# Optimization experiments

Measured on AMD Instinct MI355X. Metric: run time of the kernel, lower is better.

The kernel has to match this reference:

```python
import jax, jax.numpy as jnp
import numpy as np

D_MODEL = 1024
EPS = 1e-6

def setup_inputs() -> dict:
    key = jax.random.key(0)
    ks = jax.random.split(key, 13)
    B, T, S, E = 4, 2048, 2048, D_MODEL
    s = 1.0 / np.sqrt(E)
    return {
        "query": jax.random.normal(ks[0], (B, T, E), jnp.float32),
        "key": jax.random.normal(ks[1], (B, S, E), jnp.float32),
        "value": jax.random.normal(ks[2], (B, S, E), jnp.float32),
        "Wq": jax.random.normal(ks[3], (E, E), jnp.float32) * s,
        "bq": jax.random.normal(ks[4], (E,), jnp.float32) * 0.01,
        "Wk": jax.random.normal(ks[5], (E, E), jnp.float32) * s,
        "bk": jax.random.normal(ks[6], (E,), jnp.float32) * 0.01,
        "Wv": jax.random.normal(ks[7], (E, E), jnp.float32) * s,
        "bv": jax.random.normal(ks[8], (E,), jnp.float32) * 0.01,
        "Wo": jax.random.normal(ks[9], (E, E), jnp.float32) * s,
        "bo": jax.random.normal(ks[10], (E,), jnp.float32) * 0.01,
        "gamma": jnp.ones((E,), jnp.float32),
        "beta": jnp.zeros((E,), jnp.float32),
    }

def reference(query, key, value, Wq, bq, Wk, bk, Wv, bv, Wo, bo, gamma, beta):
    # Note: despite the name, the original never splits heads; attention is
    # over the full d_model with scale 1/sqrt(d_model). Dropout = eval identity.
    residual = query
    q = jnp.einsum('bte,fe->btf', query, Wq) + bq   # nn.Linear: x @ W.T + b
    k = jnp.einsum('bse,fe->bsf', key, Wk) + bk
    v = jnp.einsum('bse,fe->bsf', value, Wv) + bv
    scores = jnp.einsum('bte,bse->bts', q, k) / jnp.sqrt(jnp.float32(D_MODEL))
    attn = jax.nn.softmax(scores, axis=-1)          # (B, T, S)
    ctx = jnp.einsum('bts,bse->bte', attn, v)
    out = jnp.einsum('bte,fe->btf', ctx, Wo) + bo
    out = out + residual
    mu = jnp.mean(out, axis=-1, keepdims=True)
    var = jnp.mean(jnp.square(out - mu), axis=-1, keepdims=True)
    return (out - mu) * jax.lax.rsqrt(var + EPS) * gamma + beta
```

## Files before the change

### kernel.cpp

```cpp
#include <hip/hip_runtime.h>
#include <hip/hip_bf16.h>

typedef __bf16 bf16_t;
typedef __bf16 bf16x4 __attribute__((ext_vector_type(4)));
typedef __bf16 bf16x8 __attribute__((ext_vector_type(8)));
typedef float f32x4 __attribute__((ext_vector_type(4)));

#define E_DIM 1024
#define SEQ   2048
#define NBATCH 4

#define BARR()  asm volatile("s_barrier" ::: "memory")
#define LGKM0() asm volatile("s_waitcnt lgkmcnt(0)" ::: "memory")
#define VMC6()  asm volatile("s_waitcnt vmcnt(6)" ::: "memory")
#define VMC0()  asm volatile("s_waitcnt vmcnt(0)" ::: "memory")

__global__ __launch_bounds__(256) void k_cast2(
    const float* __restrict__ q, const float* __restrict__ k, const float* __restrict__ v,
    const float* __restrict__ wq, const float* __restrict__ wk,
    const float* __restrict__ wv, const float* __restrict__ wo,
    bf16_t* __restrict__ xq, bf16_t* __restrict__ xk, bf16_t* __restrict__ xv,
    bf16_t* __restrict__ wqb, bf16_t* __restrict__ wkb,
    bf16_t* __restrict__ wvb, bf16_t* __restrict__ wob) {
  const int b = blockIdx.x;
  const float* s; bf16_t* d; long base;
  if (b < 2048)        { s = q;  d = xq;  base = (long)b * 4096; }
  else if (b < 4096)   { s = k;  d = xk;  base = (long)(b - 2048) * 4096; }
  else if (b < 6144)   { s = v;  d = xv;  base = (long)(b - 4096) * 4096; }
  else if (b < 6400)   { s = wq; d = wqb; base = (long)(b - 6144) * 4096; }
  else if (b < 6656)   { s = wk; d = wkb; base = (long)(b - 6400) * 4096; }
  else if (b < 6912)   { s = wv; d = wvb; base = (long)(b - 6656) * 4096; }
  else                 { s = wo; d = wob; base = (long)(b - 6912) * 4096; }
  const long i = base + threadIdx.x * 16;
  const f32x4 a0 = *(const f32x4*)(s + i);
  const f32x4 a1 = *(const f32x4*)(s + i + 4);
  const f32x4 a2 = *(const f32x4*)(s + i + 8);
  const f32x4 a3 = *(const f32x4*)(s + i + 12);
  bf16x8 o0, o1;
#pragma unroll
  for (int j = 0; j < 4; ++j) {
    o0[j] = (bf16_t)a0[j]; o0[4 + j] = (bf16_t)a1[j];
    o1[j] = (bf16_t)a2[j]; o1[4 + j] = (bf16_t)a3[j];
  }
  *(bf16x8*)(d + i) = o0;
  *(bf16x8*)(d + i + 8) = o1;
}

template <int OUTMODE, bool RS, bool QKV3, int REPS, int NTL>
__global__ __launch_bounds__(256, 2) void k_g13(
    const bf16_t* __restrict__ A, int lda, long sA,
    const bf16_t* __restrict__ B, int ldb, long sB,
    void* __restrict__ Cv, int ldc, long sC,
    float scale, const float* __restrict__ bias,
    const float* __restrict__ residual, int GM, int GN,
    const bf16_t* __restrict__ A1, const bf16_t* __restrict__ A2,
    const bf16_t* __restrict__ B1, const bf16_t* __restrict__ B2,
    const float* __restrict__ bias1, const float* __restrict__ bias2,
    void* __restrict__ Cv1, void* __restrict__ Cv2) {
  constexpr int ASZ   = 16384;
  constexpr int BUFSZ = 32768;
  constexpr int NT    = 1 << NTL;
  constexpr int TT    = REPS << NTL;
  extern __shared__ char smem[];

  const int tid  = threadIdx.x;
  const int lane = tid & 63;
  const int wid  = tid >> 6;
  const int wm   = wid >> 1;
  const int wn   = wid & 1;
  const int l15  = lane & 15;
  const int lq   = lane >> 4;

  const int nwg  = gridDim.x;
  const int orig = blockIdx.x;
  const int wg   = (orig & 7) * (nwg >> 3) + (orig >> 3);

  const int colk = ((tid & 7) ^ ((tid >> 3) & 7)) << 3;
  const int trow = tid >> 3;
  const int ldsw = wid << 10;

  const bf16_t *pA0, *pB0, *pA1 = nullptr, *pB1 = nullptr, *pA2 = nullptr, *pB2 = nullptr;
  int zzr0 = 0, bmr0 = 0, bnr0 = 0, zzr1 = 0, bmr1 = 0, bnr1 = 0;
  if constexpr (QKV3) {
    bmr0 = wg / GN; bnr0 = wg - bmr0 * GN;
    const long aoff = (long)(bmr0 * 128 + trow) * lda + colk;
    const long boff = (long)(bnr0 * 128 + trow) * ldb + colk;
    pA0 = A + aoff;  pA1 = A1 + aoff;  pA2 = A2 + aoff;
    pB0 = B + boff;  pB1 = B1 + boff;  pB2 = B2 + boff;
  } else {
    {
      const int g  = wg;
      zzr0 = g / (GM * GN);
      const int rm = g - zzr0 * (GM * GN);
      bmr0 = rm / GN; bnr0 = rm - bmr0 * GN;
      pA0 = A + zzr0 * sA + (long)(bmr0 * 128 + trow) * lda + colk;
      pB0 = B + zzr0 * sB + (long)(bnr0 * 128 + trow) * ldb + colk;
    }
    if constexpr (REPS >= 2) {
      const int g  = nwg + wg;
      zzr1 = g / (GM * GN);
      const int rm = g - zzr1 * (GM * GN);
      bmr1 = rm / GN; bnr1 = rm - bmr1 * GN;
      pA1 = A + zzr1 * sA + (long)(bmr1 * 128 + trow) * lda + colk;
      pB1 = B + zzr1 * sB + (long)(bnr1 * 128 + trow) * ldb + colk;
    }
  }

#define GLL(gaddr, ldsoff)                                                       \
  __builtin_amdgcn_global_load_lds(                                             \
      (const __attribute__((address_space(1))) void*)(gaddr),                   \
      (__attribute__((address_space(3))) void*)(smem + (ldsoff)), 16, 0, 0)

  auto stA = [&](int tau, int buf) {
    tau = tau < TT ? tau : TT - 1;
    const int rep = tau >> NTL;
    const bf16_t* p = (REPS == 1) ? pA0
                    : (REPS == 2) ? (rep ? pA1 : pA0)
                    : (rep == 0 ? pA0 : (rep == 1 ? pA1 : pA2));
    p += (long)(tau & (NT - 1)) * 64;
#pragma unroll
    for (int s = 0; s < 4; ++s)
      GLL(p + (long)(s * 32) * lda, buf * BUFSZ + s * 4096 + ldsw);
  };
  auto stB = [&](int tau, int buf, int half) {
    tau = tau < TT ? tau : TT - 1;
    const int rep = tau >> NTL;
    const bf16_t* p = (REPS == 1) ? pB0
                    : (REPS == 2) ? (rep ? pB1 : pB0)
                    : (rep == 0 ? pB0 : (rep == 1 ? pB1 : pB2));
    p += (long)(tau & (NT - 1)) * 64;
#pragma unroll
    for (int s = 0; s < 2; ++s)
      GLL(p + (long)(half * 64 + s * 32) * ldb,
          buf * BUFSZ + ASZ + half * 8192 + s * 4096 + ldsw);
  };

  f32x4 acc[4][4];
#pragma unroll
  for (int m = 0; m < 4; ++m)
#pragma unroll
    for (int n = 0; n < 4; ++n) acc[m][n] = (f32x4){0.f, 0.f, 0.f, 0.f};
  f32x4 rs[4];
#pragma unroll
  for (int m = 0; m < 4; ++m) rs[m] = (f32x4){0.f, 0.f, 0.f, 0.f};
  bf16x8 vones;
#pragma unroll
  for (int i = 0; i < 8; ++i) vones[i] = (bf16_t)1.0f;

  auto ldA = [&](bf16x8 (&a)[2][2], int cur, int mq) {
#pragma unroll
    for (int i = 0; i < 2; ++i) {
      const int row = wm * 64 + (mq * 2 + i) * 16 + l15;
#pragma unroll
      for (int kk = 0; kk < 2; ++kk) {
        const int byt = cur * BUFSZ + row * 128 + ((kk * 64 + lq * 16) ^ ((row & 7) << 4));
        a[i][kk] = *(const bf16x8*)(smem + byt);
      }
    }
  };
  auto ldB = [&](bf16x8 (&b)[2][2], int cur, int nq) {
#pragma unroll
    for (int n2 = 0; n2 < 2; ++n2) {
      const int row = wn * 64 + (nq * 2 + n2) * 16 + l15;
#pragma unroll
      for (int kk = 0; kk < 2; ++kk) {
        const int byt = cur * BUFSZ + ASZ + row * 128 + ((kk * 64 + lq * 16) ^ ((row & 7) << 4));
        b[n2][kk] = *(const bf16x8*)(smem + byt);
      }
    }
  };
  auto mmaq = [&](bf16x8 (&a)[2][2], bf16x8 (&b)[2][2], int mq, int nq) {
    __builtin_amdgcn_s_setprio(1);
#pragma unroll
    for (int kk = 0; kk < 2; ++kk)
#pragma unroll
      for (int i = 0; i < 2; ++i)
#pragma unroll
        for (int n2 = 0; n2 < 2; ++n2)
          acc[mq * 2 + i][nq * 2 + n2] = __builtin_amdgcn_mfma_f32_16x16x32_bf16(
              a[i][kk], b[n2][kk], acc[mq * 2 + i][nq * 2 + n2], 0, 0, 0);
    __builtin_amdgcn_s_setprio(0);
  };
  auto mmars = [&](bf16x8 (&a)[2][2], int mq) {
#pragma unroll
    for (int kk = 0; kk < 2; ++kk)
#pragma unroll
      for (int i = 0; i < 2; ++i)
        rs[mq * 2 + i] = __builtin_amdgcn_mfma_f32_16x16x32_bf16(
            a[i][kk], vones, rs[mq * 2 + i], 0, 0, 0);
  };

  stB(0, 0, 0); stB(0, 0, 1); stA(0, 0);
  stB(1, 1, 0); stA(1, 1);
  VMC6();
  BARR();

  bf16x8 a0[2][2], a1[2][2], b0[2][2], b1[2][2];
  auto tile = [&](int t, int cur) {
    ldA(a0, cur, 0); ldB(b0, cur, 0);
    stB(t + 1, cur ^ 1, 1);
    BARR(); LGKM0();
    mmaq(a0, b0, 0, 0);
    BARR();
    ldB(b1, cur, 1);
    BARR(); LGKM0();
    mmaq(a0, b1, 0, 1);
    if constexpr (RS) mmars(a0, 0);
    BARR();
    ldA(a1, cur, 1);
    stB(t + 2, cur, 0);
    BARR(); LGKM0();
    mmaq(a1, b1, 1, 1);
    BARR();
    stA(t + 2, cur);
    BARR();
    mmaq(a1, b0, 1, 0);
    if constexpr (RS) mmars(a1, 1);
    VMC6();
    BARR();
  };

#pragma unroll
  for (int rep = 0; rep < REPS; ++rep) {
    const int tb = rep << NTL;
    for (int tt = 0; tt < NT; tt += 2) {
      tile(tb + tt, 0);
      tile(tb + tt + 1, 1);
    }

    {
      int zz2, bm2, bn2;
      const float* biasp;
      void* Cvp;
      bool tr = false;
      if constexpr (QKV3) {
        zz2 = 0; bm2 = bmr0; bn2 = bnr0;
        biasp = rep == 0 ? bias : (rep == 1 ? bias1 : bias2);
        Cvp   = rep == 0 ? Cv   : (rep == 1 ? Cv1   : Cv2);
        tr = (rep == 2);
      } else {
        zz2 = (REPS >= 2 && rep) ? zzr1 : zzr0;
        bm2 = (REPS >= 2 && rep) ? bmr1 : bmr0;
        bn2 = (REPS >= 2 && rep) ? bnr1 : bnr0;
        biasp = bias; Cvp = Cv;
      }
      const int colb = bn2 * 128 + wn * 64 + l15;
      const int rowb = bm2 * 128 + wm * 64 + lq * 4;
#pragma unroll
      for (int m = 0; m < 4; ++m) {
        float inv[4];
        if constexpr (RS) {
#pragma unroll
          for (int j = 0; j < 4; ++j) inv[j] = 1.0f / rs[m][j];
        }
#pragma unroll
        for (int n = 0; n < 4; ++n) {
          const int colg = colb + n * 16;
          float bval = 0.0f;
          if constexpr (OUTMODE != 3) bval = biasp ? biasp[colg] : 0.0f;
          if (QKV3 && tr) {
            const int r0 = rowb + m * 16;
            bf16x4 pk;
#pragma unroll
            for (int j = 0; j < 4; ++j) pk[j] = (bf16_t)(acc[m][n][j] * scale + bval);
            const long bb = (long)(r0 >> 11);
            const int ss = r0 & (SEQ - 1);
            *(bf16x4*)((bf16_t*)Cvp + bb * ((long)E_DIM * SEQ) + (long)colg * SEQ + ss) = pk;
          } else {
#pragma unroll
            for (int j = 0; j < 4; ++j) {
              const int r = rowb + m * 16 + j;
              float v;
              if constexpr (OUTMODE == 3) v = __expf(acc[m][n][j] * scale);
              else v = acc[m][n][j] * scale + bval;
              if constexpr (RS) v *= inv[j];
              if (OUTMODE == 0 && residual) v += residual[(long)r * ldc + colg];
              const long idx = (long)zz2 * sC + (long)r * ldc + colg;
              if constexpr (OUTMODE == 0) ((float*)Cvp)[idx] = v;
              else ((bf16_t*)Cvp)[idx] = (bf16_t)v;
            }
          }
        }
      }
      if (rep + 1 < REPS) {
#pragma unroll
        for (int m = 0; m < 4; ++m) {
#pragma unroll
          for (int n = 0; n < 4; ++n) acc[m][n] = (f32x4){0.f, 0.f, 0.f, 0.f};
          rs[m] = (f32x4){0.f, 0.f, 0.f, 0.f};
        }
      }
    }
  }
  VMC0();
#undef GLL
}

__global__ __launch_bounds__(256) void k_layernorm(float* __restrict__ out,
                                                   const float* __restrict__ gamma,
                                                   const float* __restrict__ beta) {
  const long row = blockIdx.x;
  float* rp = out + row * 1024;
  const int t = threadIdx.x;
  const float4 v = *(const float4*)(rp + t * 4);
  float s = v.x + v.y + v.z + v.w;
#pragma unroll
  for (int o = 32; o; o >>= 1) s += __shfl_xor(s, o);
  __shared__ float red1[4], red2[4];
  const int lane = t & 63, w = t >> 6;
  if (lane == 0) red1[w] = s;
  __syncthreads();
  const float mu = (red1[0] + red1[1] + red1[2] + red1[3]) * (1.0f / 1024.0f);
  const float d0 = v.x - mu, d1 = v.y - mu, d2 = v.z - mu, d3 = v.w - mu;
  float ss = d0 * d0 + d1 * d1 + d2 * d2 + d3 * d3;
#pragma unroll
  for (int o = 32; o; o >>= 1) ss += __shfl_xor(ss, o);
  if (lane == 0) red2[w] = ss;
  __syncthreads();
  const float var = (red2[0] + red2[1] + red2[2] + red2[3]) * (1.0f / 1024.0f);
  const float rsq = rsqrtf(var + 1e-6f);
  const float4 g = *(const float4*)(gamma + t * 4);
  const float4 b = *(const float4*)(beta + t * 4);
  float4 o;
  o.x = d0 * rsq * g.x + b.x;
  o.y = d1 * rsq * g.y + b.y;
  o.z = d2 * rsq * g.z + b.z;
  o.w = d3 * rsq * g.w + b.w;
  *(float4*)(rp + t * 4) = o;
}

extern "C" void kernel_launch(void* const* d_in, const int* in_sizes, int n_in,
                              void* d_out, int out_size, void* d_ws, size_t ws_size,
                              hipStream_t stream) {
  const float* query = (const float*)d_in[0];
  const float* key   = (const float*)d_in[1];
  const float* value = (const float*)d_in[2];
  const float* Wq = (const float*)d_in[3];
  const float* bq = (const float*)d_in[4];
  const float* Wk = (const float*)d_in[5];
  const float* bk = (const float*)d_in[6];
  const float* Wv = (const float*)d_in[7];
  const float* bv = (const float*)d_in[8];
  const float* Wo = (const float*)d_in[9];
  const float* bo = (const float*)d_in[10];
  const float* gamma = (const float*)d_in[11];
  const float* beta  = (const float*)d_in[12];
  float* out = (float*)d_out;

  char* ws = (char*)d_ws;
  const size_t XSZ = (size_t)NBATCH * SEQ * E_DIM * 2;
  const size_t WSZ = (size_t)E_DIM * E_DIM * 2;
  const size_t B2  = 3 * XSZ;

  bf16_t* Xq  = (bf16_t*)(ws + 0);
  bf16_t* Xk  = (bf16_t*)(ws + XSZ);
  bf16_t* Xv  = (bf16_t*)(ws + 2 * XSZ);
  bf16_t* SC  = (bf16_t*)(ws + 0);
  bf16_t* Wqb = (bf16_t*)(ws + B2);
  bf16_t* Wkb = (bf16_t*)(ws + B2 + WSZ);
  bf16_t* Wvb = (bf16_t*)(ws + B2 + 2 * WSZ);
  bf16_t* Wob = (bf16_t*)(ws + B2 + 3 * WSZ);
  bf16_t* Qb  = (bf16_t*)(ws + B2 + 4 * WSZ);
  bf16_t* Kb  = (bf16_t*)(ws + B2 + 4 * WSZ + XSZ);
  bf16_t* Vt  = (bf16_t*)(ws + B2 + 4 * WSZ + 2 * XSZ);
  bf16_t* Ctx = (bf16_t*)(ws + B2 + 4 * WSZ + 3 * XSZ);

  const int NTOK = NBATCH * SEQ;
  const int SMB = 65536;

  hipFuncSetAttribute((const void*)k_g13<1, false, true, 3, 4>, hipFuncAttributeMaxDynamicSharedMemorySize, SMB);
  hipFuncSetAttribute((const void*)k_g13<3, false, false, 2, 4>, hipFuncAttributeMaxDynamicSharedMemorySize, SMB);
  hipFuncSetAttribute((const void*)k_g13<1, true, false, 1, 5>, hipFuncAttributeMaxDynamicSharedMemorySize, SMB);
  hipFuncSetAttribute((const void*)k_g13<0, false, false, 1, 4>, hipFuncAttributeMaxDynamicSharedMemorySize, SMB);

  k_cast2<<<dim3(7168), 256, 0, stream>>>(query, key, value, Wq, Wk, Wv, Wo,
                                          Xq, Xk, Xv, Wqb, Wkb, Wvb, Wob);

  k_g13<1, false, true, 3, 4><<<512, 256, SMB, stream>>>(
      Xq, E_DIM, 0, Wqb, E_DIM, 0, Qb, E_DIM, 0, 1.0f, bq, nullptr, 64, 8,
      Xk, Xv, Wkb, Wvb, bk, bv, Kb, Vt);

  k_g13<3, false, false, 2, 4><<<512, 256, SMB, stream>>>(
      Qb, E_DIM, (long)SEQ * E_DIM, Kb, E_DIM, (long)SEQ * E_DIM,
      SC, SEQ, (long)SEQ * SEQ, 0.03125f, nullptr, nullptr, 16, 16,
      nullptr, nullptr, nullptr, nullptr, nullptr, nullptr, nullptr, nullptr);

  k_g13<1, true, false, 1, 5><<<512, 256, SMB, stream>>>(
      SC, SEQ, (long)SEQ * SEQ, Vt, SEQ, (long)E_DIM * SEQ,
      Ctx, E_DIM, (long)SEQ * E_DIM, 1.0f, nullptr, nullptr, 16, 8,
      nullptr, nullptr, nullptr, nullptr, nullptr, nullptr, nullptr, nullptr);

  k_g13<0, false, false, 1, 4><<<512, 256, SMB, stream>>>(
      Ctx, E_DIM, 0, Wob, E_DIM, 0, out, E_DIM, 0, 1.0f, bo, query, 64, 8,
      nullptr, nullptr, nullptr, nullptr, nullptr, nullptr, nullptr, nullptr);

  k_layernorm<<<dim3(NTOK), 256, 0, stream>>>(out, gamma, beta);
}
```

Measured before the change: 224.4 us.

## Pre-swizzle weights into MFMA fragment layout and load B directly to registers

The cast kernel now writes the four weight matrices in a fragment-major layout that matches the 16x16x32 MFMA B-operand ordering. A new GEMM kernel, used for the QKV projection and the output projection, loads B straight from global memory into registers each step, double-buffered, and stages only A through LDS, which halves shared memory per block. This is meant to cut LDS traffic and barrier pressure in the weight GEMMs, at the cost of more register use and direct global loads whose latency has to be hidden by the vmcnt-based pipeline.

```diff
diff --git a/kernel.cpp b/kernel.cpp
--- a/kernel.cpp
+++ b/kernel.cpp
@@ -13,6 +13,7 @@
 #define BARR()  asm volatile("s_barrier" ::: "memory")
 #define LGKM0() asm volatile("s_waitcnt lgkmcnt(0)" ::: "memory")
 #define VMC6()  asm volatile("s_waitcnt vmcnt(6)" ::: "memory")
+#define VMC12() asm volatile("s_waitcnt vmcnt(12)" ::: "memory")
 #define VMC0()  asm volatile("s_waitcnt vmcnt(0)" ::: "memory")
 
 __global__ __launch_bounds__(256) void k_cast2(
@@ -23,42 +24,63 @@
     bf16_t* __restrict__ wqb, bf16_t* __restrict__ wkb,
     bf16_t* __restrict__ wvb, bf16_t* __restrict__ wob) {
   const int b = blockIdx.x;
-  const float* s; bf16_t* d; long base;
-  if (b < 2048)        { s = q;  d = xq;  base = (long)b * 4096; }
-  else if (b < 4096)   { s = k;  d = xk;  base = (long)(b - 2048) * 4096; }
-  else if (b < 6144)   { s = v;  d = xv;  base = (long)(b - 4096) * 4096; }
-  else if (b < 6400)   { s = wq; d = wqb; base = (long)(b - 6144) * 4096; }
-  else if (b < 6656)   { s = wk; d = wkb; base = (long)(b - 6400) * 4096; }
-  else if (b < 6912)   { s = wv; d = wvb; base = (long)(b - 6656) * 4096; }
-  else                 { s = wo; d = wob; base = (long)(b - 6912) * 4096; }
-  const long i = base + threadIdx.x * 16;
-  const f32x4 a0 = *(const f32x4*)(s + i);
-  const f32x4 a1 = *(const f32x4*)(s + i + 4);
-  const f32x4 a2 = *(const f32x4*)(s + i + 8);
-  const f32x4 a3 = *(const f32x4*)(s + i + 12);
-  bf16x8 o0, o1;
-#pragma unroll
-  for (int j = 0; j < 4; ++j) {
-    o0[j] = (bf16_t)a0[j]; o0[4 + j] = (bf16_t)a1[j];
-    o1[j] = (bf16_t)a2[j]; o1[4 + j] = (bf16_t)a3[j];
+  if (b < 6144) {
+    const float* s; bf16_t* d; long base;
+    if (b < 2048)      { s = q; d = xq; base = (long)b * 4096; }
+    else if (b < 4096) { s = k; d = xk; base = (long)(b - 2048) * 4096; }
+    else               { s = v; d = xv; base = (long)(b - 4096) * 4096; }
+    const long i = base + threadIdx.x * 16;
+    const f32x4 a0 = *(const f32x4*)(s + i);
+    const f32x4 a1 = *(const f32x4*)(s + i + 4);
+    const f32x4 a2 = *(const f32x4*)(s + i + 8);
+    const f32x4 a3 = *(const f32x4*)(s + i + 12);
+    bf16x8 o0, o1;
+#pragma unroll
+    for (int j = 0; j < 4; ++j) {
+      o0[j] = (bf16_t)a0[j]; o0[4 + j] = (bf16_t)a1[j];
+      o1[j] = (bf16_t)a2[j]; o1[4 + j] = (bf16_t)a3[j];
+    }
+    *(bf16x8*)(d + i) = o0;
+    *(bf16x8*)(d + i + 8) = o1;
+  } else {
+    const int w = (b - 6144) >> 8, r = (b - 6144) & 255;
+    const float* s = (w == 0) ? wq : (w == 1) ? wk : (w == 2) ? wv : wo;
+    bf16_t* d = (w == 0) ? wqb : (w == 1) ? wkb : (w == 2) ? wvb : wob;
+    const int n  = r * 4 + (threadIdx.x >> 6);
+    const int k0 = (threadIdx.x & 63) * 16;
+    const float* sp = s + (long)n * 1024 + k0;
+    const f32x4 a0 = *(const f32x4*)(sp);
+    const f32x4 a1 = *(const f32x4*)(sp + 4);
+    const f32x4 a2 = *(const f32x4*)(sp + 8);
+    const f32x4 a3 = *(const f32x4*)(sp + 12);
+#pragma unroll
+    for (int h = 0; h < 2; ++h) {
+      const int kk = k0 + h * 8;
+      const int ln = (n & 15) + ((kk >> 3) & 3) * 16;
+      const long oi = (((long)(n >> 4) * 32 + (kk >> 5)) * 64 + ln) * 8;
+      bf16x8 o;
+#pragma unroll
+      for (int j = 0; j < 4; ++j) {
+        o[j]     = (bf16_t)(h ? a2[j] : a0[j]);
+        o[4 + j] = (bf16_t)(h ? a3[j] : a1[j]);
+      }
+      *(bf16x8*)(d + oi) = o;
+    }
   }
-  *(bf16x8*)(d + i) = o0;
-  *(bf16x8*)(d + i + 8) = o1;
 }
 
-template <int OUTMODE, bool RS, bool QKV3, int REPS, int NTL>
-__global__ __launch_bounds__(256, 2) void k_g13(
+template <int OUTMODE, bool QKV3, int REPS, int NTL>
+__global__ __launch_bounds__(256, 2) void k_g17(
     const bf16_t* __restrict__ A, int lda, long sA,
-    const bf16_t* __restrict__ B, int ldb, long sB,
+    const bf16_t* __restrict__ Bf,
     void* __restrict__ Cv, int ldc, long sC,
     float scale, const float* __restrict__ bias,
     const float* __restrict__ residual, int GM, int GN,
     const bf16_t* __restrict__ A1, const bf16_t* __restrict__ A2,
-    const bf16_t* __restrict__ B1, const bf16_t* __restrict__ B2,
+    const bf16_t* __restrict__ Bf1, const bf16_t* __restrict__ Bf2,
     const float* __restrict__ bias1, const float* __restrict__ bias2,
     void* __restrict__ Cv1, void* __restrict__ Cv2) {
-  constexpr int ASZ   = 16384;
-  constexpr int BUFSZ = 32768;
+  constexpr int BUFSZ = 16384;
   constexpr int NT    = 1 << NTL;
   constexpr int TT    = REPS << NTL;
   extern __shared__ char smem[];
@@ -79,31 +101,21 @@
   const int trow = tid >> 3;
   const int ldsw = wid << 10;
 
-  const bf16_t *pA0, *pB0, *pA1 = nullptr, *pB1 = nullptr, *pA2 = nullptr, *pB2 = nullptr;
-  int zzr0 = 0, bmr0 = 0, bnr0 = 0, zzr1 = 0, bmr1 = 0, bnr1 = 0;
+  const bf16_t *pA0, *pA1 = nullptr, *pA2 = nullptr;
+  const bf16_t *pBf0, *pBf1 = nullptr, *pBf2 = nullptr;
+  int zzr0 = 0, bmr0 = 0, bnr0 = 0;
   if constexpr (QKV3) {
     bmr0 = wg / GN; bnr0 = wg - bmr0 * GN;
     const long aoff = (long)(bmr0 * 128 + trow) * lda + colk;
-    const long boff = (long)(bnr0 * 128 + trow) * ldb + colk;
     pA0 = A + aoff;  pA1 = A1 + aoff;  pA2 = A2 + aoff;
-    pB0 = B + boff;  pB1 = B1 + boff;  pB2 = B2 + boff;
+    const long boff = ((long)(bnr0 * 8 + wn * 4) * 32 * 64 + lane) * 8;
+    pBf0 = Bf + boff;  pBf1 = Bf1 + boff;  pBf2 = Bf2 + boff;
   } else {
-    {
-      const int g  = wg;
-      zzr0 = g / (GM * GN);
-      const int rm = g - zzr0 * (GM * GN);
-      bmr0 = rm / GN; bnr0 = rm - bmr0 * GN;
-      pA0 = A + zzr0 * sA + (long)(bmr0 * 128 + trow) * lda + colk;
-      pB0 = B + zzr0 * sB + (long)(bnr0 * 128 + trow) * ldb + colk;
-    }
-    if constexpr (REPS >= 2) {
-      const int g  = nwg + wg;
-      zzr1 = g / (GM * GN);
-      const int rm = g - zzr1 * (GM * GN);
-      bmr1 = rm / GN; bnr1 = rm - bmr1 * GN;
-      pA1 = A + zzr1 * sA + (long)(bmr1 * 128 + trow) * lda + colk;
-      pB1 = B + zzr1 * sB + (long)(bnr1 * 128 + trow) * ldb + colk;
-    }
+    zzr0 = wg / (GM * GN);
+    const int rm = wg - zzr0 * (GM * GN);
+    bmr0 = rm / GN; bnr0 = rm - bmr0 * GN;
+    pA0 = A + zzr0 * sA + (long)(bmr0 * 128 + trow) * lda + colk;
+    pBf0 = Bf + ((long)(bnr0 * 8 + wn * 4) * 32 * 64 + lane) * 8;
   }
 
 #define GLL(gaddr, ldsoff)                                                       \
@@ -115,8 +127,196 @@
     tau = tau < TT ? tau : TT - 1;
     const int rep = tau >> NTL;
     const bf16_t* p = (REPS == 1) ? pA0
-                    : (REPS == 2) ? (rep ? pA1 : pA0)
                     : (rep == 0 ? pA0 : (rep == 1 ? pA1 : pA2));
+    p += (long)(tau & (NT - 1)) * 64;
+#pragma unroll
+    for (int s = 0; s < 4; ++s)
+      GLL(p + (long)(s * 32) * lda, buf * BUFSZ + s * 4096 + ldsw);
+  };
+  auto loadB = [&](bf16x8 (&Bv)[8], int tau) {
+    tau = tau < TT ? tau : TT - 1;
+    const int rep = tau >> NTL;
+    const bf16_t* p = (REPS == 1) ? pBf0
+                    : (rep == 0 ? pBf0 : (rep == 1 ? pBf1 : pBf2));
+    const int kb0 = (tau & (NT - 1)) * 2;
+#pragma unroll
+    for (int dn = 0; dn < 4; ++dn)
+#pragma unroll
+      for (int kk = 0; kk < 2; ++kk)
+        Bv[dn * 2 + kk] = *(const bf16x8*)(p + ((long)(dn * 32 + kb0 + kk)) * 512);
+  };
+
+  f32x4 acc[4][4];
+#pragma unroll
+  for (int m = 0; m < 4; ++m)
+#pragma unroll
+    for (int n = 0; n < 4; ++n) acc[m][n] = (f32x4){0.f, 0.f, 0.f, 0.f};
+
+  auto ldA = [&](bf16x8 (&a)[2][2], int cur, int mq) {
+#pragma unroll
+    for (int i = 0; i < 2; ++i) {
+      const int row = wm * 64 + (mq * 2 + i) * 16 + l15;
+#pragma unroll
+      for (int kk = 0; kk < 2; ++kk) {
+        const int byt = cur * BUFSZ + row * 128 + ((kk * 64 + lq * 16) ^ ((row & 7) << 4));
+        a[i][kk] = *(const bf16x8*)(smem + byt);
+      }
+    }
+  };
+
+  bf16x8 Bc[8], Bn[8];
+  bf16x8 a0[2][2], a1[2][2];
+
+  auto compute = [&](int cur, bf16x8 (&Bv)[8]) {
+    ldA(a0, cur, 0); ldA(a1, cur, 1);
+    __builtin_amdgcn_s_setprio(1);
+#pragma unroll
+    for (int kk = 0; kk < 2; ++kk)
+#pragma unroll
+      for (int i = 0; i < 2; ++i)
+#pragma unroll
+        for (int dn = 0; dn < 4; ++dn) {
+          acc[i][dn] = __builtin_amdgcn_mfma_f32_16x16x32_bf16(
+              a0[i][kk], Bv[dn * 2 + kk], acc[i][dn], 0, 0, 0);
+          acc[2 + i][dn] = __builtin_amdgcn_mfma_f32_16x16x32_bf16(
+              a1[i][kk], Bv[dn * 2 + kk], acc[2 + i][dn], 0, 0, 0);
+        }
+    __builtin_amdgcn_s_setprio(0);
+  };
+
+  stA(0, 0);
+  loadB(Bc, 0);
+
+#pragma unroll
+  for (int rep = 0; rep < REPS; ++rep) {
+    const int tb = rep << NTL;
+    for (int tt = 0; tt < NT; tt += 2) {
+      {
+        stA(tb + tt + 1, 1);
+        loadB(Bn, tb + tt + 1);
+        VMC12();
+        BARR();
+        compute(0, Bc);
+        BARR();
+      }
+      {
+        stA(tb + tt + 2, 0);
+        loadB(Bc, tb + tt + 2);
+        VMC12();
+        BARR();
+        compute(1, Bn);
+        BARR();
+      }
+    }
+
+    {
+      int zz2 = 0, bm2 = bmr0, bn2 = bnr0;
+      const float* biasp;
+      void* Cvp;
+      bool tr = false;
+      if constexpr (QKV3) {
+        biasp = rep == 0 ? bias : (rep == 1 ? bias1 : bias2);
+        Cvp   = rep == 0 ? Cv   : (rep == 1 ? Cv1   : Cv2);
+        tr = (rep == 2);
+      } else {
+        zz2 = zzr0; biasp = bias; Cvp = Cv;
+      }
+      const int colb = bn2 * 128 + wn * 64 + l15;
+      const int rowb = bm2 * 128 + wm * 64 + lq * 4;
+#pragma unroll
+      for (int m = 0; m < 4; ++m) {
+#pragma unroll
+        for (int n = 0; n < 4; ++n) {
+          const int colg = colb + n * 16;
+          const float bval = biasp ? biasp[colg] : 0.0f;
+          if (QKV3 && tr) {
+            const int r0 = rowb + m * 16;
+            bf16x4 pk;
+#pragma unroll
+            for (int j = 0; j < 4; ++j) pk[j] = (bf16_t)(acc[m][n][j] * scale + bval);
+            const long bb = (long)(r0 >> 11);
+            const int ss = r0 & (SEQ - 1);
+            *(bf16x4*)((bf16_t*)Cvp + bb * ((long)E_DIM * SEQ) + (long)colg * SEQ + ss) = pk;
+          } else {
+#pragma unroll
+            for (int j = 0; j < 4; ++j) {
+              const int r = rowb + m * 16 + j;
+              float v = acc[m][n][j] * scale + bval;
+              if (OUTMODE == 0 && residual) v += residual[(long)r * ldc + colg];
+              const long idx = (long)zz2 * sC + (long)r * ldc + colg;
+              if constexpr (OUTMODE == 0) ((float*)Cvp)[idx] = v;
+              else ((bf16_t*)Cvp)[idx] = (bf16_t)v;
+            }
+          }
+        }
+      }
+      if (rep + 1 < REPS) {
+#pragma unroll
+        for (int m = 0; m < 4; ++m)
+#pragma unroll
+          for (int n = 0; n < 4; ++n) acc[m][n] = (f32x4){0.f, 0.f, 0.f, 0.f};
+      }
+    }
+  }
+  VMC0();
+#undef GLL
+}
+
+template <int OUTMODE, bool RS, int REPS, int NTL>
+__global__ __launch_bounds__(256, 2) void k_g13(
+    const bf16_t* __restrict__ A, int lda, long sA,
+    const bf16_t* __restrict__ B, int ldb, long sB,
+    void* __restrict__ Cv, int ldc, long sC,
+    float scale, int GM, int GN) {
+  constexpr int ASZ   = 16384;
+  constexpr int BUFSZ = 32768;
+  constexpr int NT    = 1 << NTL;
+  constexpr int TT    = REPS << NTL;
+  extern __shared__ char smem[];
+
+  const int tid  = threadIdx.x;
+  const int lane = tid & 63;
+  const int wid  = tid >> 6;
+  const int wm   = wid >> 1;
+  const int wn   = wid & 1;
+  const int l15  = lane & 15;
+  const int lq   = lane >> 4;
+
+  const int nwg  = gridDim.x;
+  const int orig = blockIdx.x;
+  const int wg   = (orig & 7) * (nwg >> 3) + (orig >> 3);
+
+  const int colk = ((tid & 7) ^ ((tid >> 3) & 7)) << 3;
+  const int trow = tid >> 3;
+  const int ldsw = wid << 10;
+
+  const bf16_t *pA0, *pB0, *pA1 = nullptr, *pB1 = nullptr;
+  int zzr0 = 0, bmr0 = 0, bnr0 = 0, zzr1 = 0, bmr1 = 0, bnr1 = 0;
+  {
+    zzr0 = wg / (GM * GN);
+    const int rm = wg - zzr0 * (GM * GN);
+    bmr0 = rm / GN; bnr0 = rm - bmr0 * GN;
+    pA0 = A + zzr0 * sA + (long)(bmr0 * 128 + trow) * lda + colk;
+    pB0 = B + zzr0 * sB + (long)(bnr0 * 128 + trow) * ldb + colk;
+  }
+  if constexpr (REPS >= 2) {
+    const int g  = nwg + wg;
+    zzr1 = g / (GM * GN);
+    const int rm = g - zzr1 * (GM * GN);
+    bmr1 = rm / GN; bnr1 = rm - bmr1 * GN;
+    pA1 = A + zzr1 * sA + (long)(bmr1 * 128 + trow) * lda + colk;
+    pB1 = B + zzr1 * sB + (long)(bnr1 * 128 + trow) * ldb + colk;
+  }
+
+#define GLL(gaddr, ldsoff)                                                       \
+  __builtin_amdgcn_global_load_lds(                                             \
+      (const __attribute__((address_space(1))) void*)(gaddr),                   \
+      (__attribute__((address_space(3))) void*)(smem + (ldsoff)), 16, 0, 0)
+
+  auto stA = [&](int tau, int buf) {
+    tau = tau < TT ? tau : TT - 1;
+    const int rep = tau >> NTL;
+    const bf16_t* p = (REPS == 1) ? pA0 : (rep ? pA1 : pA0);
     p += (long)(tau & (NT - 1)) * 64;
 #pragma unroll
     for (int s = 0; s < 4; ++s)
@@ -125,9 +325,7 @@
   auto stB = [&](int tau, int buf, int half) {
     tau = tau < TT ? tau : TT - 1;
     const int rep = tau >> NTL;
-    const bf16_t* p = (REPS == 1) ? pB0
-                    : (REPS == 2) ? (rep ? pB1 : pB0)
-                    : (rep == 0 ? pB0 : (rep == 1 ? pB1 : pB2));
+    const bf16_t* p = (REPS == 1) ? pB0 : (rep ? pB1 : pB0);
     p += (long)(tau & (NT - 1)) * 64;
 #pragma unroll
     for (int s = 0; s < 2; ++s)
@@ -227,23 +425,10 @@
       tile(tb + tt, 0);
       tile(tb + tt + 1, 1);
     }
-
     {
-      int zz2, bm2, bn2;
-      const float* biasp;
-      void* Cvp;
-      bool tr = false;
-      if constexpr (QKV3) {
-        zz2 = 0; bm2 = bmr0; bn2 = bnr0;
-        biasp = rep == 0 ? bias : (rep == 1 ? bias1 : bias2);
-        Cvp   = rep == 0 ? Cv   : (rep == 1 ? Cv1   : Cv2);
-        tr = (rep == 2);
-      } else {
-        zz2 = (REPS >= 2 && rep) ? zzr1 : zzr0;
-        bm2 = (REPS >= 2 && rep) ? bmr1 : bmr0;
-        bn2 = (REPS >= 2 && rep) ? bnr1 : bnr0;
-        biasp = bias; Cvp = Cv;
-      }
+      const int zz2 = (REPS >= 2 && rep) ? zzr1 : zzr0;
+      const int bm2 = (REPS >= 2 && rep) ? bmr1 : bmr0;
+      const int bn2 = (REPS >= 2 && rep) ? bnr1 : bnr0;
       const int colb = bn2 * 128 + wn * 64 + l15;
       const int rowb = bm2 * 128 + wm * 64 + lq * 4;
 #pragma unroll
@@ -256,29 +441,15 @@
 #pragma unroll
         for (int n = 0; n < 4; ++n) {
           const int colg = colb + n * 16;
-          float bval = 0.0f;
-          if constexpr (OUTMODE != 3) bval = biasp ? biasp[colg] : 0.0f;
-          if (QKV3 && tr) {
-            const int r0 = rowb + m * 16;
-            bf16x4 pk;
-#pragma unroll
-            for (int j = 0; j < 4; ++j) pk[j] = (bf16_t)(acc[m][n][j] * scale + bval);
-            const long bb = (long)(r0 >> 11);
-            const int ss = r0 & (SEQ - 1);
-            *(bf16x4*)((bf16_t*)Cvp + bb * ((long)E_DIM * SEQ) + (long)colg * SEQ + ss) = pk;
-          } else {
-#pragma unroll
-            for (int j = 0; j < 4; ++j) {
-              const int r = rowb + m * 16 + j;
-              float v;
-              if constexpr (OUTMODE == 3) v = __expf(acc[m][n][j] * scale);
-              else v = acc[m][n][j] * scale + bval;
-              if constexpr (RS) v *= inv[j];
-              if (OUTMODE == 0 && residual) v += residual[(long)r * ldc + colg];
-              const long idx = (long)zz2 * sC + (long)r * ldc + colg;
-              if constexpr (OUTMODE == 0) ((float*)Cvp)[idx] = v;
-              else ((bf16_t*)Cvp)[idx] = (bf16_t)v;
-            }
+#pragma unroll
+          for (int j = 0; j < 4; ++j) {
+            const int r = rowb + m * 16 + j;
+            float v;
+            if constexpr (OUTMODE == 3) v = __expf(acc[m][n][j] * scale);
+            else v = acc[m][n][j] * scale;
+            if constexpr (RS) v *= inv[j];
+            const long idx = (long)zz2 * sC + (long)r * ldc + colg;
+            ((bf16_t*)Cv)[idx] = (bf16_t)v;
           }
         }
       }
@@ -367,31 +538,30 @@
 
   const int NTOK = NBATCH * SEQ;
   const int SMB = 65536;
-
-  hipFuncSetAttribute((const void*)k_g13<1, false, true, 3, 4>, hipFuncAttributeMaxDynamicSharedMemorySize, SMB);
-  hipFuncSetAttribute((const void*)k_g13<3, false, false, 2, 4>, hipFuncAttributeMaxDynamicSharedMemorySize, SMB);
-  hipFuncSetAttribute((const void*)k_g13<1, true, false, 1, 5>, hipFuncAttributeMaxDynamicSharedMemorySize, SMB);
-  hipFuncSetAttribute((const void*)k_g13<0, false, false, 1, 4>, hipFuncAttributeMaxDynamicSharedMemorySize, SMB);
+  const int SMB17 = 32768;
+
+  hipFuncSetAttribute((const void*)k_g17<1, true, 3, 4>,  hipFuncAttributeMaxDynamicSharedMemorySize, SMB17);
+  hipFuncSetAttribute((const void*)k_g17<0, false, 1, 4>, hipFuncAttributeMaxDynamicSharedMemorySize, SMB17);
+  hipFuncSetAttribute((const void*)k_g13<3, false, 2, 4>, hipFuncAttributeMaxDynamicSharedMemorySize, SMB);
+  hipFuncSetAttribute((const void*)k_g13<1, true, 1, 5>,  hipFuncAttributeMaxDynamicSharedMemorySize, SMB);
 
   k_cast2<<<dim3(7168), 256, 0, stream>>>(query, key, value, Wq, Wk, Wv, Wo,
                                           Xq, Xk, Xv, Wqb, Wkb, Wvb, Wob);
 
-  k_g13<1, false, true, 3, 4><<<512, 256, SMB, stream>>>(
-      Xq, E_DIM, 0, Wqb, E_DIM, 0, Qb, E_DIM, 0, 1.0f, bq, nullptr, 64, 8,
+  k_g17<1, true, 3, 4><<<512, 256, SMB17, stream>>>(
+      Xq, E_DIM, 0, Wqb, Qb, E_DIM, 0, 1.0f, bq, nullptr, 64, 8,
       Xk, Xv, Wkb, Wvb, bk, bv, Kb, Vt);
 
-  k_g13<3, false, false, 2, 4><<<512, 256, SMB, stream>>>(
+  k_g13<3, false, 2, 4><<<512, 256, SMB, stream>>>(
       Qb, E_DIM, (long)SEQ * E_DIM, Kb, E_DIM, (long)SEQ * E_DIM,
-      SC, SEQ, (long)SEQ * SEQ, 0.03125f, nullptr, nullptr, 16, 16,
-      nullptr, nullptr, nullptr, nullptr, nullptr, nullptr, nullptr, nullptr);
-
-  k_g13<1, true, false, 1, 5><<<512, 256, SMB, stream>>>(
+      SC, SEQ, (long)SEQ * SEQ, 0.03125f, 16, 16);
+
+  k_g13<1, true, 1, 5><<<512, 256, SMB, stream>>>(
       SC, SEQ, (long)SEQ * SEQ, Vt, SEQ, (long)E_DIM * SEQ,
-      Ctx, E_DIM, (long)SEQ * E_DIM, 1.0f, nullptr, nullptr, 16, 8,
-      nullptr, nullptr, nullptr, nullptr, nullptr, nullptr, nullptr, nullptr);
-
-  k_g13<0, false, false, 1, 4><<<512, 256, SMB, stream>>>(
-      Ctx, E_DIM, 0, Wob, E_DIM, 0, out, E_DIM, 0, 1.0f, bo, query, 64, 8,
+      Ctx, E_DIM, (long)SEQ * E_DIM, 1.0f, 16, 8);
+
+  k_g17<0, false, 1, 4><<<512, 256, SMB17, stream>>>(
+      Ctx, E_DIM, 0, Wob, out, E_DIM, 0, 1.0f, bo, query, 64, 8,
       nullptr, nullptr, nullptr, nullptr, nullptr, nullptr, nullptr, nullptr);
 
   k_layernorm<<<dim3(NTOK), 256, 0, stream>>>(out, gamma, beta);
```

Measured after the change: 234.4 us. 4.4% more time.

## Split each 128x128 GEMM tile across eight waves instead of four

Applied to the files above, without the earlier changes.

The GEMM kernel now launches 512 threads per block, arranged as a 2x4 wave grid. Each wave computes a 64x32 sub-tile instead of 64x64, which halves the accumulator registers per wave. The global-to-LDS copy loops and the vmcnt waits are scaled to the larger thread count. The aim is more resident waves per CU to hide memory and LDS latency. The cost is more LDS fragment reads per MFMA, since A fragments are now shared across four waves, and more barrier participants.

```diff
diff --git a/kernel.cpp b/kernel.cpp
--- a/kernel.cpp
+++ b/kernel.cpp
@@ -12,7 +12,7 @@
 
 #define BARR()  asm volatile("s_barrier" ::: "memory")
 #define LGKM0() asm volatile("s_waitcnt lgkmcnt(0)" ::: "memory")
-#define VMC6()  asm volatile("s_waitcnt vmcnt(6)" ::: "memory")
+#define VMC3()  asm volatile("s_waitcnt vmcnt(3)" ::: "memory")
 #define VMC0()  asm volatile("s_waitcnt vmcnt(0)" ::: "memory")
 
 __global__ __launch_bounds__(256) void k_cast2(
@@ -47,7 +47,7 @@
 }
 
 template <int OUTMODE, bool RS, bool QKV3, int REPS, int NTL>
-__global__ __launch_bounds__(256, 2) void k_g13(
+__global__ __launch_bounds__(512, 2) void k_g19(
     const bf16_t* __restrict__ A, int lda, long sA,
     const bf16_t* __restrict__ B, int ldb, long sB,
     void* __restrict__ Cv, int ldc, long sC,
@@ -66,8 +66,8 @@
   const int tid  = threadIdx.x;
   const int lane = tid & 63;
   const int wid  = tid >> 6;
-  const int wm   = wid >> 1;
-  const int wn   = wid & 1;
+  const int wm   = wid >> 2;
+  const int wn   = wid & 3;
   const int l15  = lane & 15;
   const int lq   = lane >> 4;
 
@@ -119,8 +119,8 @@
                     : (rep == 0 ? pA0 : (rep == 1 ? pA1 : pA2));
     p += (long)(tau & (NT - 1)) * 64;
 #pragma unroll
-    for (int s = 0; s < 4; ++s)
-      GLL(p + (long)(s * 32) * lda, buf * BUFSZ + s * 4096 + ldsw);
+    for (int s = 0; s < 2; ++s)
+      GLL(p + (long)(s * 64) * lda, buf * BUFSZ + s * 8192 + ldsw);
   };
   auto stB = [&](int tau, int buf, int half) {
     tau = tau < TT ? tau : TT - 1;
@@ -129,17 +129,14 @@
                     : (REPS == 2) ? (rep ? pB1 : pB0)
                     : (rep == 0 ? pB0 : (rep == 1 ? pB1 : pB2));
     p += (long)(tau & (NT - 1)) * 64;
-#pragma unroll
-    for (int s = 0; s < 2; ++s)
-      GLL(p + (long)(half * 64 + s * 32) * ldb,
-          buf * BUFSZ + ASZ + half * 8192 + s * 4096 + ldsw);
-  };
-
-  f32x4 acc[4][4];
+    GLL(p + (long)(half * 64) * ldb, buf * BUFSZ + ASZ + half * 8192 + ldsw);
+  };
+
+  f32x4 acc[4][2];
 #pragma unroll
   for (int m = 0; m < 4; ++m)
 #pragma unroll
-    for (int n = 0; n < 4; ++n) acc[m][n] = (f32x4){0.f, 0.f, 0.f, 0.f};
+    for (int n = 0; n < 2; ++n) acc[m][n] = (f32x4){0.f, 0.f, 0.f, 0.f};
   f32x4 rs[4];
 #pragma unroll
   for (int m = 0; m < 4; ++m) rs[m] = (f32x4){0.f, 0.f, 0.f, 0.f};
@@ -158,27 +155,22 @@
       }
     }
   };
-  auto ldB = [&](bf16x8 (&b)[2][2], int cur, int nq) {
-#pragma unroll
-    for (int n2 = 0; n2 < 2; ++n2) {
-      const int row = wn * 64 + (nq * 2 + n2) * 16 + l15;
-#pragma unroll
-      for (int kk = 0; kk < 2; ++kk) {
-        const int byt = cur * BUFSZ + ASZ + row * 128 + ((kk * 64 + lq * 16) ^ ((row & 7) << 4));
-        b[n2][kk] = *(const bf16x8*)(smem + byt);
-      }
-    }
-  };
-  auto mmaq = [&](bf16x8 (&a)[2][2], bf16x8 (&b)[2][2], int mq, int nq) {
+  auto ldB = [&](bf16x8 (&b)[2], int cur, int nq) {
+    const int row = wn * 32 + nq * 16 + l15;
+#pragma unroll
+    for (int kk = 0; kk < 2; ++kk) {
+      const int byt = cur * BUFSZ + ASZ + row * 128 + ((kk * 64 + lq * 16) ^ ((row & 7) << 4));
+      b[kk] = *(const bf16x8*)(smem + byt);
+    }
+  };
+  auto mmaq = [&](bf16x8 (&a)[2][2], bf16x8 (&b)[2], int mq, int nq) {
     __builtin_amdgcn_s_setprio(1);
 #pragma unroll
     for (int kk = 0; kk < 2; ++kk)
 #pragma unroll
       for (int i = 0; i < 2; ++i)
-#pragma unroll
-        for (int n2 = 0; n2 < 2; ++n2)
-          acc[mq * 2 + i][nq * 2 + n2] = __builtin_amdgcn_mfma_f32_16x16x32_bf16(
-              a[i][kk], b[n2][kk], acc[mq * 2 + i][nq * 2 + n2], 0, 0, 0);
+        acc[mq * 2 + i][nq] = __builtin_amdgcn_mfma_f32_16x16x32_bf16(
+            a[i][kk], b[kk], acc[mq * 2 + i][nq], 0, 0, 0);
     __builtin_amdgcn_s_setprio(0);
   };
   auto mmars = [&](bf16x8 (&a)[2][2], int mq) {
@@ -192,10 +184,10 @@
 
   stB(0, 0, 0); stB(0, 0, 1); stA(0, 0);
   stB(1, 1, 0); stA(1, 1);
-  VMC6();
+  VMC3();
   BARR();
 
-  bf16x8 a0[2][2], a1[2][2], b0[2][2], b1[2][2];
+  bf16x8 a0[2][2], a1[2][2], b0[2], b1[2];
   auto tile = [&](int t, int cur) {
     ldA(a0, cur, 0); ldB(b0, cur, 0);
     stB(t + 1, cur ^ 1, 1);
@@ -216,7 +208,7 @@
     BARR();
     mmaq(a1, b0, 1, 0);
     if constexpr (RS) mmars(a1, 1);
-    VMC6();
+    VMC3();
     BARR();
   };
 
@@ -244,7 +236,7 @@
         bn2 = (REPS >= 2 && rep) ? bnr1 : bnr0;
         biasp = bias; Cvp = Cv;
       }
-      const int colb = bn2 * 128 + wn * 64 + l15;
+      const int colb = bn2 * 128 + wn * 32 + l15;
       const int rowb = bm2 * 128 + wm * 64 + lq * 4;
 #pragma unroll
       for (int m = 0; m < 4; ++m) {
@@ -254,7 +246,7 @@
           for (int j = 0; j < 4; ++j) inv[j] = 1.0f / rs[m][j];
         }
 #pragma unroll
-        for (int n = 0; n < 4; ++n) {
+        for (int n = 0; n < 2; ++n) {
           const int colg = colb + n * 16;
           float bval = 0.0f;
           if constexpr (OUTMODE != 3) bval = biasp ? biasp[colg] : 0.0f;
@@ -286,7 +278,7 @@
 #pragma unroll
         for (int m = 0; m < 4; ++m) {
 #pragma unroll
-          for (int n = 0; n < 4; ++n) acc[m][n] = (f32x4){0.f, 0.f, 0.f, 0.f};
+          for (int n = 0; n < 2; ++n) acc[m][n] = (f32x4){0.f, 0.f, 0.f, 0.f};
           rs[m] = (f32x4){0.f, 0.f, 0.f, 0.f};
         }
       }
@@ -368,29 +360,29 @@
   const int NTOK = NBATCH * SEQ;
   const int SMB = 65536;
 
-  hipFuncSetAttribute((const void*)k_g13<1, false, true, 3, 4>, hipFuncAttributeMaxDynamicSharedMemorySize, SMB);
-  hipFuncSetAttribute((const void*)k_g13<3, false, false, 2, 4>, hipFuncAttributeMaxDynamicSharedMemorySize, SMB);
-  hipFuncSetAttribute((const void*)k_g13<1, true, false, 1, 5>, hipFuncAttributeMaxDynamicSharedMemorySize, SMB);
-  hipFuncSetAttribute((const void*)k_g13<0, false, false, 1, 4>, hipFuncAttributeMaxDynamicSharedMemorySize, SMB);
+  hipFuncSetAttribute((const void*)k_g19<1, false, true, 3, 4>, hipFuncAttributeMaxDynamicSharedMemorySize, SMB);
+  hipFuncSetAttribute((const void*)k_g19<3, false, false, 2, 4>, hipFuncAttributeMaxDynamicSharedMemorySize, SMB);
+  hipFuncSetAttribute((const void*)k_g19<1, true, false, 1, 5>, hipFuncAttributeMaxDynamicSharedMemorySize, SMB);
+  hipFuncSetAttribute((const void*)k_g19<0, false, false, 1, 4>, hipFuncAttributeMaxDynamicSharedMemorySize, SMB);
 
   k_cast2<<<dim3(7168), 256, 0, stream>>>(query, key, value, Wq, Wk, Wv, Wo,
                                           Xq, Xk, Xv, Wqb, Wkb, Wvb, Wob);
 
-  k_g13<1, false, true, 3, 4><<<512, 256, SMB, stream>>>(
+  k_g19<1, false, true, 3, 4><<<512, 512, SMB, stream>>>(
       Xq, E_DIM, 0, Wqb, E_DIM, 0, Qb, E_DIM, 0, 1.0f, bq, nullptr, 64, 8,
       Xk, Xv, Wkb, Wvb, bk, bv, Kb, Vt);
 
-  k_g13<3, false, false, 2, 4><<<512, 256, SMB, stream>>>(
+  k_g19<3, false, false, 2, 4><<<512, 512, SMB, stream>>>(
       Qb, E_DIM, (long)SEQ * E_DIM, Kb, E_DIM, (long)SEQ * E_DIM,
       SC, SEQ, (long)SEQ * SEQ, 0.03125f, nullptr, nullptr, 16, 16,
       nullptr, nullptr, nullptr, nullptr, nullptr, nullptr, nullptr, nullptr);
 
-  k_g13<1, true, false, 1, 5><<<512, 256, SMB, stream>>>(
+  k_g19<1, true, false, 1, 5><<<512, 512, SMB, stream>>>(
       SC, SEQ, (long)SEQ * SEQ, Vt, SEQ, (long)E_DIM * SEQ,
       Ctx, E_DIM, (long)SEQ * E_DIM, 1.0f, nullptr, nullptr, 16, 8,
       nullptr, nullptr, nullptr, nullptr, nullptr, nullptr, nullptr, nullptr);
 
-  k_g13<0, false, false, 1, 4><<<512, 256, SMB, stream>>>(
+  k_g19<0, false, false, 1, 4><<<512, 512, SMB, stream>>>(
       Ctx, E_DIM, 0, Wob, E_DIM, 0, out, E_DIM, 0, 1.0f, bo, query, 64, 8,
       nullptr, nullptr, nullptr, nullptr, nullptr, nullptr, nullptr, nullptr);
 
```

Result: no change. 228.7 us (+1.9%).
